# Kernel tuning notes

Hardware: AMD Instinct MI355X
Metric: run time of the kernel (lower is better)

The kernel has to match this reference:

```python
import jax, jax.numpy as jnp
import numpy as np

B, T, H = 1024, 512, 256  # batch, seq_len, hidden_layer_size; input_size=1, output_size=1


def setup_inputs() -> dict:
    key = jax.random.key(0)
    ks = jax.random.split(key, 7)
    s = 1.0 / np.sqrt(H)  # PyTorch LSTM/Linear init scale (uniform bound); normal here, scaled similarly
    return {
        "input_seq": jax.random.normal(ks[0], (B, T), dtype=jnp.float32),
        "W_ih": jax.random.normal(ks[1], (4 * H, 1), dtype=jnp.float32) * s,
        "W_hh": jax.random.normal(ks[2], (4 * H, H), dtype=jnp.float32) * s,
        "b_ih": jax.random.normal(ks[3], (4 * H,), dtype=jnp.float32) * s,
        "b_hh": jax.random.normal(ks[4], (4 * H,), dtype=jnp.float32) * s,
        "W_lin": jax.random.normal(ks[5], (1, H), dtype=jnp.float32) * s,
        "b_lin": jax.random.normal(ks[6], (1,), dtype=jnp.float32) * s,
    }


def _lstm_last_hidden(x, W_ih, W_hh, b_ih, b_hh):
    # x: [B, T] scalar series -> treated as [B, T, 1] (input_size = 1).
    # Precompute the input projection for all timesteps at once:
    # xg[b, t, :] = x[b, t] * W_ih[:, 0] + b_ih + b_hh   -> [B, T, 4H]
    xg = x[:, :, None] * W_ih[:, 0] + (b_ih + b_hh)
    xg = jnp.swapaxes(xg, 0, 1)  # [T, B, 4H] for scan over time

    h0 = jnp.zeros((x.shape[0], H), dtype=x.dtype)
    c0 = jnp.zeros((x.shape[0], H), dtype=x.dtype)

    def step(carry, xg_t):
        h, c = carry
        gates = xg_t + h @ W_hh.T  # [B, 4H]
        i, f, g, o = jnp.split(gates, 4, axis=-1)  # PyTorch gate order: i, f, g, o
        i = jax.nn.sigmoid(i)
        f = jax.nn.sigmoid(f)
        g = jnp.tanh(g)
        o = jax.nn.sigmoid(o)
        c = f * c + i * g
        h = o * jnp.tanh(c)
        return (h, c), None

    (h_n, _), _ = jax.lax.scan(step, (h0, c0), xg)
    return h_n  # [B, H]


def reference(input_seq, W_ih, W_hh, b_ih, b_hh, W_lin, b_lin):
    h_n = _lstm_last_hidden(input_seq, W_ih, W_hh, b_ih, b_hh)
    predictions = h_n @ W_lin.T + b_lin  # [B, 1]
    return predictions
```

## Files before the change

kernel.cpp:

```cpp
#include <hip/hip_runtime.h>


#define HID 256
#define TT 512
#define BROWS 16
#define NBLK 64
#define THREADS 512
#define HPAD 264

typedef float v4f __attribute__((ext_vector_type(4)));
typedef unsigned int v4u __attribute__((ext_vector_type(4)));
typedef __bf16 v8bf __attribute__((ext_vector_type(8)));

__device__ __forceinline__ unsigned short f2bf(float f) {
    unsigned int u = __builtin_bit_cast(unsigned int, f);
    u += 0x7fffu + ((u >> 16) & 1u);
    return (unsigned short)(u >> 16);
}
__device__ __forceinline__ float bf2f(unsigned short s) {
    unsigned int u = ((unsigned int)s) << 16;
    return __builtin_bit_cast(float, u);
}
__device__ __forceinline__ float fsigmoid(float x) {
    float e = exp2f(x * -1.44269504f);
    return __builtin_amdgcn_rcpf(1.0f + e);
}
__device__ __forceinline__ float ftanh(float x) {
    float e = exp2f(x * 2.88539008f);
    return 1.0f - 2.0f * __builtin_amdgcn_rcpf(1.0f + e);
}

__global__ void wconv_kernel(const float* __restrict__ Whh,
                             unsigned short* __restrict__ Wbf) {
    int tid = blockIdx.x * blockDim.x + threadIdx.x;
    int lane = tid & 63;
    int frag = tid >> 6;
    int Tn = frag >> 3;
    int kc = frag & 7;
    int n  = Tn * 16 + (lane & 15);
    int kb = kc * 32 + (lane >> 4) * 8;
    const float* src = Whh + (size_t)n * HID + kb;
    unsigned short* dst = Wbf + (size_t)tid * 8;
#pragma unroll
    for (int j = 0; j < 8; ++j) dst[j] = f2bf(src[j]);
}

#define MFMA8(ACC, BARR, BOFF)                                               \
    _Pragma("unroll")                                                        \
    for (int kc = 0; kc < 8; ++kc)                                           \
        ACC = __builtin_amdgcn_mfma_f32_16x16x32_bf16(afrag[kc],             \
                  BARR[(BOFF) + kc], ACC, 0, 0, 0);

#define LDSTILE(ACC, SLOT)                                                   \
    { v8bf bl_[8];                                                           \
      _Pragma("unroll")                                                      \
      for (int kc = 0; kc < 8; ++kc)                                         \
          bl_[kc] = __builtin_bit_cast(v8bf, *(const v4u*)(Wlds +            \
                      ((size_t)(((SLOT) * 8 + kc) * 64 + lane)) * 8));       \
      MFMA8(ACC, bl_, 0) }

#define SLOADT(SB, TN)                                                       \
    _Pragma("unroll")                                                        \
    for (int kc = 0; kc < 8; ++kc)                                           \
        SB[kc] = __builtin_bit_cast(v8bf, *(const v4u*)(Wbf +                \
                   ((size_t)((TN) * 8 + kc) * 64 + lane) * 8));

#define INITG(S, AI, AF, AG, AO)                                             \
    { int nb = 16 * (w + 8 * (S)) + l4;                                      \
      float w0 = gw[nb],       b0 = gb[nb];                                  \
      float w1 = gw[256 + nb], b1 = gb[256 + nb];                            \
      float w2 = gw[512 + nb], b2 = gb[512 + nb];                            \
      float w3 = gw[768 + nb], b3 = gb[768 + nb];                            \
      _Pragma("unroll")                                                      \
      for (int r = 0; r < 4; ++r) {                                          \
          AI[r] = xv[r] * w0 + b0; AF[r] = xv[r] * w1 + b1;                  \
          AG[r] = xv[r] * w2 + b2; AO[r] = xv[r] * w3 + b3; } }

#define GATES(S, AI, AF, AG, AO)                                             \
    _Pragma("unroll")                                                        \
    for (int r = 0; r < 4; ++r) {                                            \
        float gi = fsigmoid(AI[r]);                                          \
        float gf = fsigmoid(AF[r]);                                          \
        float gg = ftanh(AG[r]);                                             \
        float go = fsigmoid(AO[r]);                                          \
        float cn = gf * c_st[(S) * 4 + r] + gi * gg;                         \
        c_st[(S) * 4 + r] = cn;                                              \
        hn_[(quad * 4 + r) * HPAD + 16 * (w + 8 * (S)) + l4] =               \
            f2bf(go * ftanh(cn));                                            \
    }

__global__ __launch_bounds__(THREADS, 2)
void lstm_kernel(const float* __restrict__ x,
                 const float* __restrict__ W_ih,
                 const float* __restrict__ b_ih,
                 const float* __restrict__ b_hh,
                 const float* __restrict__ W_lin,
                 const float* __restrict__ b_lin,
                 const unsigned short* __restrict__ Wbf,
                 float* __restrict__ out) {
    __shared__ __align__(16) unsigned short Wlds[16 * 8 * 64 * 8];
    __shared__ __align__(16) unsigned short hbuf[2][BROWS * HPAD];
    __shared__ float gw[1024];
    __shared__ float gb[1024];
    __shared__ float part[THREADS];

    const int tid  = threadIdx.x;
    const int lane = tid & 63;
    const int w    = tid >> 6;
    const int l4   = lane & 15;
    const int quad = lane >> 4;
    const int r0   = blockIdx.x * BROWS;

    for (int i = tid; i < 1024; i += THREADS) {
        gw[i] = W_ih[i];
        gb[i] = b_ih[i] + b_hh[i];
    }
    for (int i = tid; i < BROWS * HPAD; i += THREADS) hbuf[0][i] = 0;

    v8bf wres[32];
#pragma unroll
    for (int S = 0; S < 2; ++S)
#pragma unroll
        for (int G = 0; G < 2; ++G) {
            int Tn = 16 * G + w + 8 * S;
#pragma unroll
            for (int kc = 0; kc < 8; ++kc)
                wres[(S * 2 + G) * 8 + kc] = __builtin_bit_cast(v8bf,
                    *(const v4u*)(Wbf + ((size_t)(Tn * 8 + kc) * 64 + lane) * 8));
        }
#pragma unroll
    for (int S = 0; S < 2; ++S) {
        int Tn = 32 + w + 8 * S;
        int slot = w * 2 + S;
#pragma unroll
        for (int kc = 0; kc < 8; ++kc) {
            v4u d = *(const v4u*)(Wbf + ((size_t)(Tn * 8 + kc) * 64 + lane) * 8);
            *(v4u*)(Wlds + ((size_t)((slot * 8 + kc) * 64 + lane)) * 8) = d;
        }
    }
    __syncthreads();

    float c_st[8];
#pragma unroll
    for (int i = 0; i < 8; ++i) c_st[i] = 0.0f;

    v8bf sb[8];
    SLOADT(sb, 48 + w)

    int cur = 0;
    for (int t = 0; t < TT; ++t) {
        const unsigned short* hb = hbuf[cur];
        unsigned short* hn_ = hbuf[cur ^ 1];

        float xv[4];
#pragma unroll
        for (int r = 0; r < 4; ++r)
            xv[r] = x[(size_t)(r0 + quad * 4 + r) * TT + t];

        v8bf afrag[8];
        const unsigned short* hrow = hb + l4 * HPAD + quad * 8;
#pragma unroll
        for (int kc = 0; kc < 8; ++kc)
            afrag[kc] = __builtin_bit_cast(v8bf, *(const v4u*)(hrow + kc * 32));

        {
            v4f ai, af2, ag, ao;
            INITG(0, ai, af2, ag, ao)
            MFMA8(ai, wres, 0)
            MFMA8(af2, wres, 8)
            LDSTILE(ag, w * 2 + 0)
            MFMA8(ao, sb, 0)
            SLOADT(sb, 56 + w)
            GATES(0, ai, af2, ag, ao)
        }
        {
            v4f ai, af2, ag, ao;
            INITG(1, ai, af2, ag, ao)
            MFMA8(ai, wres, 16)
            MFMA8(af2, wres, 24)
            LDSTILE(ag, w * 2 + 1)
            MFMA8(ao, sb, 0)
            SLOADT(sb, 48 + w)
            GATES(1, ai, af2, ag, ao)
        }

        cur ^= 1;
        __syncthreads();
    }

    {
        int rrow = tid >> 5, s5 = tid & 31;
        float p = 0.0f;
#pragma unroll
        for (int jj = 0; jj < 8; ++jj) {
            int j = s5 * 8 + jj;
            p += bf2f(hbuf[cur][rrow * HPAD + j]) * W_lin[j];
        }
        part[tid] = p;
    }
    __syncthreads();
    if (tid < 16) {
        float sum = 0.0f;
#pragma unroll
        for (int s = 0; s < 32; ++s) sum += part[tid * 32 + s];
        out[r0 + tid] = sum + b_lin[0];
    }
}

extern "C" void kernel_launch(void* const* d_in, const int* in_sizes, int n_in,
                              void* d_out, int out_size, void* d_ws, size_t ws_size,
                              hipStream_t stream) {
    const float* x     = (const float*)d_in[0];
    const float* W_ih  = (const float*)d_in[1];
    const float* W_hh  = (const float*)d_in[2];
    const float* b_ih  = (const float*)d_in[3];
    const float* b_hh  = (const float*)d_in[4];
    const float* W_lin = (const float*)d_in[5];
    const float* b_lin = (const float*)d_in[6];
    unsigned short* Wbf = (unsigned short*)d_ws;

    wconv_kernel<<<128, 256, 0, stream>>>(W_hh, Wbf);
    lstm_kernel<<<NBLK, THREADS, 0, stream>>>(x, W_ih, b_ih, b_hh, W_lin, b_lin,
                                              Wbf, (float*)d_out);
}
```

Measured before the change: 1.584 ms.

## Stream global W tiles with rolling prefetch, XOR-swizzle h buffer, prefetch x

Replaces the full 8-fragment global prefetch of the streamed o-gate tile with a 4-deep rolling buffer that issues each load right after the MFMA that frees its slot, and moves the streamed tile first in the schedule. The padded hidden-state LDS layout is replaced by an XOR swizzle to avoid bank conflicts without padding. The input x for the next step is prefetched one step ahead, and __syncthreads is replaced by an inline waitcnt+barrier that skips the vmcnt wait. This lowers register pressure and load latency exposure, at the cost of relying on the hand-written barrier not waiting on outstanding global loads.

```diff
diff --git a/kernel.cpp b/kernel.cpp
--- a/kernel.cpp
+++ b/kernel.cpp
@@ -6,7 +6,6 @@
 #define BROWS 16
 #define NBLK 64
 #define THREADS 512
-#define HPAD 264
 
 typedef float v4f __attribute__((ext_vector_type(4)));
 typedef unsigned int v4u __attribute__((ext_vector_type(4)));
@@ -59,11 +58,13 @@
                       ((size_t)(((SLOT) * 8 + kc) * 64 + lane)) * 8));       \
       MFMA8(ACC, bl_, 0) }
 
-#define SLOADT(SB, TN)                                                       \
+#define STREAMTILE(ACC, SO, OBASE)                                           \
     _Pragma("unroll")                                                        \
-    for (int kc = 0; kc < 8; ++kc)                                           \
-        SB[kc] = __builtin_bit_cast(v8bf, *(const v4u*)(Wbf +                \
-                   ((size_t)((TN) * 8 + kc) * 64 + lane) * 8));
+    for (int kc = 0; kc < 8; ++kc) {                                         \
+        ACC = __builtin_amdgcn_mfma_f32_16x16x32_bf16(afrag[kc],             \
+                  SO[kc & 3], ACC, 0, 0, 0);                                 \
+        SO[kc & 3] = __builtin_bit_cast(v8bf, OBASE[((kc + 4) & 7) * 64]);   \
+    }
 
 #define INITG(S, AI, AF, AG, AO)                                             \
     { int nb = 16 * (w + 8 * (S)) + l4;                                      \
@@ -77,17 +78,19 @@
           AG[r] = xv[r] * w2 + b2; AO[r] = xv[r] * w3 + b3; } }
 
 #define GATES(S, AI, AF, AG, AO)                                             \
-    _Pragma("unroll")                                                        \
-    for (int r = 0; r < 4; ++r) {                                            \
+    { int n_ = 16 * (w + 8 * (S)) + l4;                                      \
+      int gn = n_ >> 3;                                                      \
+      _Pragma("unroll")                                                      \
+      for (int r = 0; r < 4; ++r) {                                          \
         float gi = fsigmoid(AI[r]);                                          \
         float gf = fsigmoid(AF[r]);                                          \
         float gg = ftanh(AG[r]);                                             \
         float go = fsigmoid(AO[r]);                                          \
         float cn = gf * c_st[(S) * 4 + r] + gi * gg;                         \
         c_st[(S) * 4 + r] = cn;                                              \
-        hn_[(quad * 4 + r) * HPAD + 16 * (w + 8 * (S)) + l4] =               \
-            f2bf(go * ftanh(cn));                                            \
-    }
+        int m = quad * 4 + r;                                                \
+        hn_[m * 256 + ((gn ^ m) & 31) * 8 + (n_ & 7)] = f2bf(go * ftanh(cn));\
+      } }
 
 __global__ __launch_bounds__(THREADS, 2)
 void lstm_kernel(const float* __restrict__ x,
@@ -99,7 +102,7 @@
                  const unsigned short* __restrict__ Wbf,
                  float* __restrict__ out) {
     __shared__ __align__(16) unsigned short Wlds[16 * 8 * 64 * 8];
-    __shared__ __align__(16) unsigned short hbuf[2][BROWS * HPAD];
+    __shared__ __align__(16) unsigned short hbuf[2][BROWS * 256];
     __shared__ float gw[1024];
     __shared__ float gb[1024];
     __shared__ float part[THREADS];
@@ -115,86 +118,101 @@
         gw[i] = W_ih[i];
         gb[i] = b_ih[i] + b_hh[i];
     }
-    for (int i = tid; i < BROWS * HPAD; i += THREADS) hbuf[0][i] = 0;
+    for (int i = tid; i < BROWS * 256; i += THREADS) {
+        hbuf[0][i] = 0;
+        hbuf[1][i] = 0;
+    }
+
+    const v4u* __restrict__ Wv = (const v4u*)Wbf;
 
     v8bf wres[32];
-#pragma unroll
-    for (int S = 0; S < 2; ++S)
-#pragma unroll
-        for (int G = 0; G < 2; ++G) {
-            int Tn = 16 * G + w + 8 * S;
+    {
+        const int tns[4] = {w, 16 + w, 8 + w, 24 + w};
+#pragma unroll
+        for (int qq = 0; qq < 4; ++qq)
 #pragma unroll
             for (int kc = 0; kc < 8; ++kc)
-                wres[(S * 2 + G) * 8 + kc] = __builtin_bit_cast(v8bf,
-                    *(const v4u*)(Wbf + ((size_t)(Tn * 8 + kc) * 64 + lane) * 8));
-        }
+                wres[qq * 8 + kc] = __builtin_bit_cast(v8bf,
+                    Wv[((size_t)(tns[qq]) * 8 + kc) * 64 + lane]);
+    }
 #pragma unroll
     for (int S = 0; S < 2; ++S) {
         int Tn = 32 + w + 8 * S;
         int slot = w * 2 + S;
 #pragma unroll
         for (int kc = 0; kc < 8; ++kc) {
-            v4u d = *(const v4u*)(Wbf + ((size_t)(Tn * 8 + kc) * 64 + lane) * 8);
+            v4u d = Wv[((size_t)Tn * 8 + kc) * 64 + lane];
             *(v4u*)(Wlds + ((size_t)((slot * 8 + kc) * 64 + lane)) * 8) = d;
         }
     }
     __syncthreads();
 
+    const v4u* __restrict__ ob0 = Wv + ((size_t)(48 + w) * 8) * 64 + lane;
+    const v4u* __restrict__ ob1 = Wv + ((size_t)(56 + w) * 8) * 64 + lane;
+    v8bf so0[4], so1[4];
+#pragma unroll
+    for (int j = 0; j < 4; ++j) {
+        so0[j] = __builtin_bit_cast(v8bf, ob0[j * 64]);
+        so1[j] = __builtin_bit_cast(v8bf, ob1[j * 64]);
+    }
+
     float c_st[8];
 #pragma unroll
     for (int i = 0; i < 8; ++i) c_st[i] = 0.0f;
 
-    v8bf sb[8];
-    SLOADT(sb, 48 + w)
+    v4f xv;
+#pragma unroll
+    for (int r = 0; r < 4; ++r)
+        xv[r] = x[(size_t)(r0 + quad * 4 + r) * TT];
 
     int cur = 0;
     for (int t = 0; t < TT; ++t) {
         const unsigned short* hb = hbuf[cur];
         unsigned short* hn_ = hbuf[cur ^ 1];
 
-        float xv[4];
-#pragma unroll
-        for (int r = 0; r < 4; ++r)
-            xv[r] = x[(size_t)(r0 + quad * 4 + r) * TT + t];
-
         v8bf afrag[8];
-        const unsigned short* hrow = hb + l4 * HPAD + quad * 8;
 #pragma unroll
         for (int kc = 0; kc < 8; ++kc)
-            afrag[kc] = __builtin_bit_cast(v8bf, *(const v4u*)(hrow + kc * 32));
+            afrag[kc] = __builtin_bit_cast(v8bf, *(const v4u*)(
+                hb + l4 * 256 + (((kc * 4 + quad) ^ l4) & 31) * 8));
 
         {
             v4f ai, af2, ag, ao;
             INITG(0, ai, af2, ag, ao)
+            STREAMTILE(ao, so0, ob0)
             MFMA8(ai, wres, 0)
             MFMA8(af2, wres, 8)
             LDSTILE(ag, w * 2 + 0)
-            MFMA8(ao, sb, 0)
-            SLOADT(sb, 56 + w)
             GATES(0, ai, af2, ag, ao)
         }
         {
             v4f ai, af2, ag, ao;
             INITG(1, ai, af2, ag, ao)
+            {
+                int tn = (t + 1 < TT) ? (t + 1) : t;
+#pragma unroll
+                for (int r = 0; r < 4; ++r)
+                    xv[r] = x[(size_t)(r0 + quad * 4 + r) * TT + tn];
+            }
+            STREAMTILE(ao, so1, ob1)
             MFMA8(ai, wres, 16)
             MFMA8(af2, wres, 24)
             LDSTILE(ag, w * 2 + 1)
-            MFMA8(ao, sb, 0)
-            SLOADT(sb, 48 + w)
             GATES(1, ai, af2, ag, ao)
         }
 
+        asm volatile("s_waitcnt lgkmcnt(0)\n\ts_barrier" ::: "memory");
         cur ^= 1;
-        __syncthreads();
     }
 
     {
         int rrow = tid >> 5, s5 = tid & 31;
+        int pos = (s5 ^ rrow) & 31;
         float p = 0.0f;
 #pragma unroll
         for (int jj = 0; jj < 8; ++jj) {
             int j = s5 * 8 + jj;
-            p += bf2f(hbuf[cur][rrow * HPAD + j]) * W_lin[j];
+            p += bf2f(hbuf[cur][rrow * 256 + pos * 8 + jj]) * W_lin[j];
         }
         part[tid] = p;
     }
```

After: 1.861 ms. +17.5%, slower.
